# Performance work log

Hardware: AMD Instinct MI355X
Metric: run time of the kernel (lower is better)

Reference implementation:

```python
import jax, jax.numpy as jnp
import numpy as np

B_, S_, F_, N_, H_ = 4, 8192, 512, 64, 2048  # batch, seq, features, state_dim, mlp hidden
EPS = 1e-5


def setup_inputs() -> dict:
    key = jax.random.key(0)
    ks = jax.random.split(key, 24)
    F, N, H = F_, N_, H_

    def nrm(k, shape, scale=1.0):
        return jax.random.normal(k, shape, dtype=jnp.float32) * scale

    inp = {}
    inp['x'] = nrm(ks[0], (B_, S_, F))
    inp['cond'] = nrm(ks[1], (B_, F))
    n = jnp.arange(N, dtype=jnp.float32)
    for i, p in enumerate(['fwd', 'bwd']):
        b = 2 + i * 6
        inp[p + '_logAre'] = jnp.log(n + 0.5)          # HiPPO-diag: A_real = -(n+0.5)
        inp[p + '_Aim'] = jnp.pi * n                    # HiPPO-diag: A_imag = pi*n
        inp[p + '_Bre'] = nrm(ks[b], (N, F), 1.0 / np.sqrt(N))
        inp[p + '_Bim'] = nrm(ks[b + 1], (N, F), 1.0 / np.sqrt(N))
        inp[p + '_Cre'] = nrm(ks[b + 2], (F, N), 1.0 / np.sqrt(F))
        inp[p + '_Cim'] = nrm(ks[b + 3], (F, N), 1.0 / np.sqrt(F))
        inp[p + '_D'] = nrm(ks[b + 4], (F,))
        inp[p + '_logdt'] = jax.random.uniform(ks[b + 5], (N,), minval=jnp.log(0.001), maxval=jnp.log(0.1))
    inp['proj_w'] = nrm(ks[14], (2 * F, F), 1.0 / np.sqrt(2 * F))
    inp['proj_b'] = jnp.zeros((F,), jnp.float32)
    # AdaLN modulation: Dense(6F) on silu(cond); zero-init in the model, small random here
    inp['ada_w'] = nrm(ks[15], (F, 6 * F), 0.02)
    inp['ada_b'] = jnp.zeros((6 * F,), jnp.float32)
    inp['mlp_w1'] = nrm(ks[16], (F, H), 1.0 / np.sqrt(F))
    inp['mlp_b1'] = jnp.zeros((H,), jnp.float32)
    inp['mlp_w2'] = nrm(ks[17], (H, F), 1.0 / np.sqrt(H))
    inp['mlp_b2'] = jnp.zeros((F,), jnp.float32)
    return inp


def _ln(x):
    mu = jnp.mean(x, axis=-1, keepdims=True)
    v = jnp.mean(jnp.square(x - mu), axis=-1, keepdims=True)
    return (x - mu) * jax.lax.rsqrt(v + EPS)


def _s5(u, logAre, Aim, Bre, Bim, Cre, Cim, D, logdt):
    dt = jnp.exp(logdt)
    A = -jnp.exp(logAre) + 1j * Aim                       # [N] complex diagonal
    A_bar = jnp.exp(A * dt)                               # ZOH discretization
    B_bar = (A_bar[:, None] - 1.0) / (A[:, None] + 1e-8) * (Bre + 1j * Bim)  # [N,F]
    u32 = u.astype(jnp.float32)
    Bu = jnp.einsum('bsf,nf->bsn', u32, B_bar)            # [B,S,N] complex
    Ab = jnp.broadcast_to(A_bar[None, None, :], Bu.shape)

    def op(e1, e2):
        a1, b1 = e1
        a2, b2 = e2
        return (a1 * a2, a2 * b1 + b2)

    _, xs = jax.lax.associative_scan(op, (Ab, Bu), axis=1)
    y = jnp.einsum('fn,bsn->bsf', Cre + 1j * Cim, xs).real + D * u32
    return y.astype(u.dtype)


def reference(x, cond, fwd_logAre, fwd_Aim, fwd_Bre, fwd_Bim, fwd_Cre, fwd_Cim, fwd_D, fwd_logdt,
              bwd_logAre, bwd_Aim, bwd_Bre, bwd_Bim, bwd_Cre, bwd_Cim, bwd_D, bwd_logdt,
              proj_w, proj_b, ada_w, ada_b, mlp_w1, mlp_b1, mlp_w2, mlp_b2):
    mods = jax.nn.silu(cond) @ ada_w + ada_b              # [B,6F]
    sh1, sc1, g1, sh2, sc2, g2 = [m[:, None, :] for m in jnp.split(mods, 6, axis=-1)]
    h = _ln(x) * (1.0 + sc1) + sh1
    y_fwd = _s5(h, fwd_logAre, fwd_Aim, fwd_Bre, fwd_Bim, fwd_Cre, fwd_Cim, fwd_D, fwd_logdt)
    y_bwd = jnp.flip(_s5(jnp.flip(h, axis=1), bwd_logAre, bwd_Aim, bwd_Bre, bwd_Bim, bwd_Cre, bwd_Cim, bwd_D, bwd_logdt), axis=1)
    y = jnp.concatenate([y_fwd, y_bwd], axis=-1) @ proj_w + proj_b
    x = x + g1 * y
    h2 = _ln(x) * (1.0 + sc2) + sh2
    x = x + g2 * (jax.nn.gelu(h2 @ mlp_w1 + mlp_b1) @ mlp_w2 + mlp_b2)
    return x
```

## Files before the change

kernel.cpp:

```cpp
#include <hip/hip_runtime.h>
#include <hip/hip_bf16.h>

typedef unsigned short u16;
typedef __attribute__((ext_vector_type(8))) short bf16x8;
typedef __attribute__((ext_vector_type(4))) float f32x4;

#define Bc 4
#define Sc 8192
#define Fc 512
#define Nc 64
#define Hc 2048
#define Tc 32768
#define SIXF 3072

__device__ __forceinline__ u16 f2bf(float v) {
  __hip_bfloat16 h = __float2bfloat16(v);
  return *reinterpret_cast<u16*>(&h);
}
__device__ __forceinline__ float bf2f(u16 u) {
  return __uint_as_float(((unsigned)u) << 16);
}
__device__ __forceinline__ float ldf(const void* p, long i, int bf) {
  return bf ? bf2f(((const u16*)p)[i]) : ((const float*)p)[i];
}

__device__ __forceinline__ void ld16(const u16* g, u16* l) {
  __builtin_amdgcn_global_load_lds(
      (const __attribute__((address_space(1))) unsigned int*)g,
      (__attribute__((address_space(3))) unsigned int*)l,
      16, 0, 0);
}

__device__ __forceinline__ void xcd_swz(int& bx, int& by) {
  int gx = gridDim.x;
  int nwg = gx * gridDim.y;
  int lin = blockIdx.x + gx * blockIdx.y;
  if ((nwg & 7) == 0) {
    int q = nwg >> 3;
    lin = (lin & 7) * q + (lin >> 3);
  }
  bx = lin % gx;
  by = lin / gx;
}

__global__ void k_detect(const u16* __restrict__ x, int* __restrict__ flag) {
  if (threadIdx.x == 0) {
    int cnt = 0;
    for (int i = 0; i < 256; ++i) {
      int e = (x[i] >> 7) & 0xFF;
      cnt += (e >= 130);
    }
    *flag = (cnt >= 16) ? 0 : 1;
  }
}

__global__ void k_convert(const void* __restrict__ src, float* __restrict__ dst,
                          int n, const int* __restrict__ flag) {
  int bf = *flag;
  int i = blockIdx.x * blockDim.x + threadIdx.x;
  int stride = gridDim.x * blockDim.x;
  for (int j = i; j < n; j += stride) dst[j] = ldf(src, j, bf);
}

__global__ __launch_bounds__(256) void k_mods_init(const void* __restrict__ ada_b,
                                                   const int* __restrict__ flag,
                                                   float* __restrict__ mods) {
  int bf = *flag;
  int col = blockIdx.x * 256 + threadIdx.x;
  float v = ldf(ada_b, col, bf);
  for (int b = 0; b < Bc; ++b) mods[b * SIXF + col] = v;
}

__global__ __launch_bounds__(256) void k_mods2(const void* __restrict__ cond,
                                               const void* __restrict__ ada_w,
                                               const int* __restrict__ flag,
                                               float* __restrict__ mods) {
  int bf = *flag;
  int b = blockIdx.y;
  int f0 = blockIdx.z * 128;
  int col = blockIdx.x * 256 + threadIdx.x;
  __shared__ float sc[128];
  for (int i = threadIdx.x; i < 128; i += 256) {
    float c = ldf(cond, b * Fc + f0 + i, bf);
    sc[i] = c / (1.f + expf(-c));
  }
  __syncthreads();
  float acc = 0.f;
  for (int f = 0; f < 128; ++f) acc = fmaf(sc[f], ldf(ada_w, (long)(f0 + f) * SIXF + col, bf), acc);
  atomicAdd(&mods[b * SIXF + col], acc);
}

__global__ void k_prep(const void* lAf, const void* Aif, const void* Brf, const void* Bif, const void* ldtf,
                       const void* lAb, const void* Aib, const void* Brb, const void* Bib, const void* ldtb,
                       const int* __restrict__ flag,
                       u16* __restrict__ Wbup, float* __restrict__ Abar) {
  int bf = *flag;
  int dir = blockIdx.x;
  int f0 = blockIdx.y * 64;
  int n = threadIdx.x;
  const void* lA = dir ? lAb : lAf;
  const void* Ai = dir ? Aib : Aif;
  const void* Br = dir ? Brb : Brf;
  const void* Bi = dir ? Bib : Bif;
  const void* ld = dir ? ldtb : ldtf;
  float dt  = expf(ldf(ld, n, bf));
  float Are = -expf(ldf(lA, n, bf));
  float Aim = ldf(Ai, n, bf);
  float er  = expf(Are * dt);
  float abr = er * cosf(Aim * dt);
  float abi = er * sinf(Aim * dt);
  if (blockIdx.y == 0) {
    Abar[(dir * Nc + n) * 2 + 0] = abr;
    Abar[(dir * Nc + n) * 2 + 1] = abi;
  }
  float dr = Are + 1e-8f, di = Aim;
  float den = dr * dr + di * di;
  float nr = abr - 1.f, ni = abi;
  float cr = (nr * dr + ni * di) / den;
  float ci = (ni * dr - nr * di) / den;
  int col_re = dir * 128 + n, col_im = dir * 128 + 64 + n;
  for (int f = f0; f < f0 + 64; ++f) {
    float br = ldf(Br, n * Fc + f, bf), bi = ldf(Bi, n * Fc + f, bf);
    Wbup[(((f >> 3) * 256) + col_re) * 8 + (f & 7)] = f2bf(cr * br - ci * bi);
    Wbup[(((f >> 3) * 256) + col_im) * 8 + (f & 7)] = f2bf(cr * bi + ci * br);
  }
}

__global__ __launch_bounds__(256) void k_P2p(const void* Df, const void* Db, const void* pw,
                                             const int* __restrict__ flag, u16* __restrict__ P2p) {
  int bf = *flag;
  int idx = blockIdx.x * 256 + threadIdx.x;
  int f1 = idx >> 9, fo = idx & 511;
  float v = ldf(Df, f1, bf) * ldf(pw, (long)f1 * Fc + fo, bf) +
            ldf(Db, f1, bf) * ldf(pw, (long)(Fc + f1) * Fc + fo, bf);
  P2p[(((f1 >> 3) * Fc) + fo) * 8 + (f1 & 7)] = f2bf(v);
}

__global__ __launch_bounds__(256) void k_Cpm(const void* Cref, const void* Cimf,
                                             const void* Creb, const void* Cimb,
                                             const int* __restrict__ flag, u16* __restrict__ Cpm) {
  int bf = *flag;
  int k = blockIdx.x;
  int dir = k >> 7, c = (k >> 6) & 1, n = k & 63;
  const void* C = dir ? (c ? Cimb : Creb) : (c ? Cimf : Cref);
  float sgn = c ? -1.f : 1.f;
  for (int f = threadIdx.x; f < Fc; f += 256)
    Cpm[k * Fc + f] = f2bf(sgn * ldf(C, (long)f * Nc + n, bf));
}

__global__ __launch_bounds__(256) void k_Wpack(const void* __restrict__ src, const int* __restrict__ flag,
                                               int log2N, u16* __restrict__ dst) {
  int bf = *flag;
  long i = (long)blockIdx.x * 256 + threadIdx.x;
  int Nn = 1 << log2N;
  long k8 = i >> log2N;
  int n = (int)(i & (Nn - 1));
  u16 tmp[8];
#pragma unroll
  for (int j = 0; j < 8; ++j)
    tmp[j] = f2bf(ldf(src, ((k8 << 3) + j) * (long)Nn + n, bf));
  *(ushort4*)(dst + i * 8)     = *(ushort4*)tmp;
  *(ushort4*)(dst + i * 8 + 4) = *(ushort4*)(tmp + 4);
}

__global__ __launch_bounds__(256) void k_ln(const void* __restrict__ src, int srcmode,
                                            long src_tok_base, int b0,
                                            const int* __restrict__ flag,
                                            const float* __restrict__ mods,
                                            int sh_base, int sc_base,
                                            u16* __restrict__ dst) {
  int bf = srcmode ? 1 : *flag;
  long lt = blockIdx.x;
  int b = b0 + (int)(lt >> 13);
  int t = threadIdx.x;
  long si = (src_tok_base + lt) * Fc;
  float x0 = ldf(src, si + t, bf);
  float x1 = ldf(src, si + t + 256, bf);
  float s = x0 + x1, qq = x0 * x0 + x1 * x1;
  for (int o = 32; o; o >>= 1) { s += __shfl_down(s, o); qq += __shfl_down(qq, o); }
  __shared__ float ss[4], sq[4];
  int w = t >> 6;
  if ((t & 63) == 0) { ss[w] = s; sq[w] = qq; }
  __syncthreads();
  float S = ss[0] + ss[1] + ss[2] + ss[3];
  float Q = sq[0] + sq[1] + sq[2] + sq[3];
  float mu = S * (1.f / Fc);
  float var = Q * (1.f / Fc) - mu * mu;
  float rs = rsqrtf(var + 1e-5f);
  const float* mb = mods + b * SIXF;
  float h0 = (x0 - mu) * rs * (1.f + mb[sc_base + t]) + mb[sh_base + t];
  float h1 = (x1 - mu) * rs * (1.f + mb[sc_base + t + 256]) + mb[sh_base + t + 256];
  dst[lt * Fc + t] = f2bf(h0);
  dst[lt * Fc + t + 256] = f2bf(h1);
}

struct Smem { u16 As[2][128 * 64]; u16 Ws[2][64 * 128]; };

__device__ __forceinline__ int mfma_gemm(Smem& sm, int cur,
                                         const u16* __restrict__ A, long row0, int K,
                                         const u16* __restrict__ Wp, int N, int col0,
                                         f32x4 (&acc)[4][4]) {
  const int tid = threadIdx.x;
  const int l = tid & 63;
  const int q = l >> 4, li = l & 15;
  const int w = tid >> 6;
  const int wm = (w >> 1) << 6, wn = (w & 1) << 6;
  const int m0 = tid >> 3;
  const int kc0 = (tid & 7) ^ (m0 & 7);
  const long aoff0 = (row0 + m0) * (long)K + (kc0 << 3);
  const long woff0 = (long)(tid >> 7) * ((long)N << 3) + ((long)(col0 + (tid & 127)) << 3);
  const int lbase = w << 9;
  const int T = K >> 6;

  auto stage = [&](int buf, int k0) {
#pragma unroll
    for (int it = 0; it < 4; ++it)
      ld16(A + aoff0 + (long)it * ((long)K << 5) + k0, sm.As[buf] + lbase + (it << 11));
#pragma unroll
    for (int it = 0; it < 4; ++it)
      ld16(Wp + woff0 + (long)k0 * N + (long)it * ((long)N << 4), sm.Ws[buf] + lbase + (it << 11));
  };

  stage(cur, 0);
  asm volatile("s_waitcnt vmcnt(0)" ::: "memory");
  __builtin_amdgcn_s_barrier();
  __builtin_amdgcn_sched_barrier(0);

  for (int t = 0; t < T; ++t) {
    if (t + 1 < T) stage(cur ^ 1, (t + 1) << 6);
    const u16* As = sm.As[cur];
    const u16* Ws = sm.Ws[cur];
#pragma unroll
    for (int ks = 0; ks < 2; ++ks) {
      bf16x8 af[4], bw[4];
#pragma unroll
      for (int mt = 0; mt < 4; ++mt) {
        int mrow = wm + (mt << 4) + li;
        af[mt] = *(const bf16x8*)(As + (((mrow << 3) + (((ks << 2) + q) ^ (mrow & 7))) << 3));
      }
#pragma unroll
      for (int nt = 0; nt < 4; ++nt) {
        int n = wn + (nt << 4) + li;
        bw[nt] = *(const bf16x8*)(Ws + ((((((ks << 2) + q) << 7) + n)) << 3));
      }
#pragma unroll
      for (int mt = 0; mt < 4; ++mt)
#pragma unroll
        for (int nt = 0; nt < 4; ++nt)
          acc[mt][nt] = __builtin_amdgcn_mfma_f32_16x16x32_bf16(af[mt], bw[nt], acc[mt][nt], 0, 0, 0);
    }
    if (t + 1 < T) {
      asm volatile("s_waitcnt vmcnt(0)" ::: "memory");
      __builtin_amdgcn_s_barrier();
      __builtin_amdgcn_sched_barrier(0);
    }
    cur ^= 1;
  }
  return cur;
}

__global__ __launch_bounds__(256) void k_Gp2(const u16* __restrict__ Cpm, const u16* __restrict__ pwp,
                                             u16* __restrict__ Gp) {
  __shared__ Smem sm;
  f32x4 acc[4][4] = {};
  int bx, by; xcd_swz(bx, by);
  long row0 = (long)by * 128;
  int col0 = bx << 7;
  int dir = (int)(row0 >> 7);
  mfma_gemm(sm, 0, Cpm, row0, Fc, pwp + (size_t)dir * 262144, Fc, col0, acc);
  const int l = threadIdx.x & 63, q = l >> 4, li = l & 15;
  const int w = threadIdx.x >> 6;
  const int wm = (w >> 1) << 6, wn = (w & 1) << 6;
#pragma unroll
  for (int mt = 0; mt < 4; ++mt)
#pragma unroll
    for (int nt = 0; nt < 4; ++nt)
#pragma unroll
      for (int r = 0; r < 4; ++r) {
        int k = (int)row0 + wm + (mt << 4) + (q << 2) + r;
        int col = col0 + wn + (nt << 4) + li;
        Gp[(((k >> 3) * Fc) + col) * 8 + (k & 7)] = f2bf(acc[mt][nt][r]);
      }
}

__global__ __launch_bounds__(256) void k_gemm_bu(const u16* __restrict__ h,
                                                 const u16* __restrict__ Wbup,
                                                 int nb, float* __restrict__ Bu) {
  __shared__ Smem sm;
  f32x4 acc[4][4] = {};
  int bx, by; xcd_swz(bx, by);
  long row0 = (long)by * 128;
  int col0 = bx << 7;
  mfma_gemm(sm, 0, h, row0, Fc, Wbup, 256, col0, acc);
  const int l = threadIdx.x & 63, q = l >> 4, li = l & 15;
  const int w = threadIdx.x >> 6;
  const int wm = (w >> 1) << 6, wn = (w & 1) << 6;
#pragma unroll
  for (int mt = 0; mt < 4; ++mt) {
#pragma unroll
    for (int nt = 0; nt < 4; ++nt) {
      int col = col0 + wn + (nt << 4) + li;
      int dir = col >> 7, cc = (col >> 6) & 1, n = col & 63;
#pragma unroll
      for (int r = 0; r < 4; ++r) {
        long lt = row0 + wm + (mt << 4) + (q << 2) + r;
        int lb = (int)(lt >> 13), s = (int)(lt & 8191);
        int spos = dir ? (Sc - 1 - s) : s;
        Bu[((((long)dir * nb + lb) * Nc + n) * Sc + spos) * 2 + cc] = acc[mt][nt][r];
      }
    }
  }
}

__global__ __launch_bounds__(256) void k_scan(float* __restrict__ Bu, const float* __restrict__ Abar,
                                              int nb) {
  int blk = blockIdx.x;
  int per_dir = nb * 64;
  int dir = blk / per_dir;
  int rem = blk - dir * per_dir;
  int lb = rem >> 6, n = rem & 63;
  float ar = Abar[(dir * Nc + n) * 2 + 0];
  float ai = Abar[(dir * Nc + n) * 2 + 1];
  float* base = Bu + (((long)dir * nb + lb) * Nc + n) * Sc * 2;
  int t = threadIdx.x;
  float4 loc[16];
  float lr = 0.f, li = 0.f;
  const float4* bp = (const float4*)base + t * 16;
#pragma unroll
  for (int j = 0; j < 16; ++j) {
    float4 v = bp[j];
    loc[j] = v;
    float nr = fmaf(ar, lr, fmaf(-ai, li, v.x));
    float ni = fmaf(ar, li, fmaf(ai, lr, v.y));
    lr = fmaf(ar, nr, fmaf(-ai, ni, v.z));
    li = fmaf(ar, ni, fmaf(ai, nr, v.w));
  }
  __shared__ float sr[256], si[256];
  float pr = ar, pi = ai;
  for (int k = 0; k < 5; ++k) { float t2 = pr * pr - pi * pi; pi = 2.f * pr * pi; pr = t2; }
  float vr = lr, vi = li;
  for (int step = 1; step < 256; step <<= 1) {
    sr[t] = vr; si[t] = vi;
    __syncthreads();
    if (t >= step) {
      float orr = sr[t - step], oii = si[t - step];
      vr = vr + pr * orr - pi * oii;
      vi = vi + pr * oii + pi * orr;
    }
    __syncthreads();
    float t2 = pr * pr - pi * pi; pi = 2.f * pr * pi; pr = t2;
  }
  sr[t] = vr; si[t] = vi;
  __syncthreads();
  float xr = (t == 0) ? 0.f : sr[t - 1];
  float xi = (t == 0) ? 0.f : si[t - 1];
  float4* op = (float4*)base + t * 16;
#pragma unroll
  for (int j = 0; j < 16; ++j) {
    float4 v = loc[j];
    float nr = fmaf(ar, xr, fmaf(-ai, xi, v.x));
    float ni = fmaf(ar, xi, fmaf(ai, xr, v.y));
    xr = fmaf(ar, nr, fmaf(-ai, ni, v.z));
    xi = fmaf(ar, ni, fmaf(ai, nr, v.w));
    float4 o; o.x = nr; o.y = ni; o.z = xr; o.w = xi;
    op[j] = o;
  }
}

__global__ __launch_bounds__(256) void k_xs_t(const float* __restrict__ xs, int nb,
                                              u16* __restrict__ xh, u16* __restrict__ xl) {
  __shared__ float tile[32 * 257];
  long t0 = (long)blockIdx.x * 32;
  int lb = (int)(t0 >> 13);
  int s0 = (int)(t0 & 8191);
  int tid = threadIdx.x;
  int ls = tid & 31;
  int half = (tid >> 5) & 1;
  int wv = tid >> 6;
#pragma unroll 4
  for (int cg = 0; cg < 32; ++cg) {
    int col = cg * 8 + wv * 2 + half;
    int dir = col >> 7, cc = (col >> 6) & 1, n = col & 63;
    int spos = dir ? (Sc - 1 - (s0 + ls)) : (s0 + ls);
    float v = xs[((((long)dir * nb + lb) * Nc + n) * Sc + spos) * 2 + cc];
    tile[ls * 257 + col] = v;
  }
  __syncthreads();
  for (int j = 0; j < 32; ++j) {
    float v = tile[j * 257 + tid];
    u16 hi = f2bf(v);
    long lt = t0 + j;
    xh[lt * 256 + tid] = hi;
    xl[lt * 256 + tid] = f2bf(v - bf2f(hi));
  }
}

__global__ __launch_bounds__(256) void k_gemm_y(const u16* __restrict__ xh, const u16* __restrict__ xl,
                                                const u16* __restrict__ Gp,
                                                const u16* __restrict__ h, const u16* __restrict__ P2p,
                                                const void* __restrict__ xraw, long tok_base, int b0,
                                                const int* __restrict__ flag,
                                                const float* __restrict__ mods, const float* __restrict__ pb,
                                                u16* __restrict__ out1) {
  __shared__ Smem sm;
  f32x4 acc[4][4] = {};
  int bx, by; xcd_swz(bx, by);
  long row0 = (long)by * 128;
  int col0 = bx << 7;
  int cur = 0;
  cur = mfma_gemm(sm, cur, xh, row0, 256, Gp, Fc, col0, acc);
  cur = mfma_gemm(sm, cur, xl, row0, 256, Gp, Fc, col0, acc);
  cur = mfma_gemm(sm, cur, h, row0, Fc, P2p, Fc, col0, acc);
  int bf = *flag;
  const int l = threadIdx.x & 63, q = l >> 4, li = l & 15;
  const int w = threadIdx.x >> 6;
  const int wm = (w >> 1) << 6, wn = (w & 1) << 6;
#pragma unroll
  for (int mt = 0; mt < 4; ++mt) {
#pragma unroll
    for (int r = 0; r < 4; ++r) {
      long lt = row0 + wm + (mt << 4) + (q << 2) + r;
      int b = b0 + (int)(lt >> 13);
      const float* mb = mods + b * SIXF + 2 * Fc;
#pragma unroll
      for (int nt = 0; nt < 4; ++nt) {
        int col = col0 + wn + (nt << 4) + li;
        float xv = ldf(xraw, (tok_base + lt) * Fc + col, bf);
        out1[lt * Fc + col] = f2bf(xv + mb[col] * (acc[mt][nt][r] + pb[col]));
      }
    }
  }
}

__device__ __forceinline__ float gelu_t(float u) {
  float z = 0.7978845608028654f * fmaf(0.044715f * u * u, u, u);
  float e = __builtin_amdgcn_exp2f(z * -2.8853900817779268f);
  return u * __builtin_amdgcn_rcpf(1.f + e);
}

__global__ __launch_bounds__(256) void k_mlp1(const u16* __restrict__ h2, const u16* __restrict__ W1p,
                                              const float* __restrict__ b1, long crow0,
                                              u16* __restrict__ tbuf) {
  __shared__ Smem sm;
  f32x4 acc[4][4] = {};
  int bx, by; xcd_swz(bx, by);
  long row0 = crow0 + (long)by * 128;
  int col0 = bx << 7;
  mfma_gemm(sm, 0, h2, row0, Fc, W1p, Hc, col0, acc);
  const int l = threadIdx.x & 63, q = l >> 4, li = l & 15;
  const int w = threadIdx.x >> 6;
  const int wm = (w >> 1) << 6, wn = (w & 1) << 6;
#pragma unroll
  for (int mt = 0; mt < 4; ++mt) {
#pragma unroll
    for (int r = 0; r < 4; ++r) {
      long lr2 = row0 - crow0 + wm + (mt << 4) + (q << 2) + r;
#pragma unroll
      for (int nt = 0; nt < 4; ++nt) {
        int col = col0 + wn + (nt << 4) + li;
        tbuf[lr2 * Hc + col] = f2bf(gelu_t(acc[mt][nt][r] + b1[col]));
      }
    }
  }
}

__global__ __launch_bounds__(256) void k_mlp2(const u16* __restrict__ tbuf, const u16* __restrict__ W2p,
                                              const float* __restrict__ b2, const u16* __restrict__ out1,
                                              const float* __restrict__ mods, long crow0,
                                              long tok_base, int b0,
                                              const int* __restrict__ flag, void* __restrict__ dout) {
  __shared__ Smem sm;
  f32x4 acc[4][4] = {};
  int bx, by; xcd_swz(bx, by);
  long lrow0 = (long)by * 128;
  int col0 = bx << 7;
  mfma_gemm(sm, 0, tbuf, lrow0, Hc, W2p, Fc, col0, acc);
  int bf = *flag;
  const int l = threadIdx.x & 63, q = l >> 4, li = l & 15;
  const int w = threadIdx.x >> 6;
  const int wm = (w >> 1) << 6, wn = (w & 1) << 6;
#pragma unroll
  for (int mt = 0; mt < 4; ++mt) {
#pragma unroll
    for (int r = 0; r < 4; ++r) {
      long lt = crow0 + lrow0 + wm + (mt << 4) + (q << 2) + r;
      int b = b0 + (int)(lt >> 13);
      const float* mb = mods + b * SIXF + 5 * Fc;
#pragma unroll
      for (int nt = 0; nt < 4; ++nt) {
        int col = col0 + wn + (nt << 4) + li;
        float v = bf2f(out1[lt * Fc + col]) + mb[col] * (acc[mt][nt][r] + b2[col]);
        long oi = (tok_base + lt) * Fc + col;
        if (bf) ((u16*)dout)[oi] = f2bf(v);
        else    ((float*)dout)[oi] = v;
      }
    }
  }
}

extern "C" void kernel_launch(void* const* d_in, const int* in_sizes, int n_in,
                              void* d_out, int out_size, void* d_ws, size_t ws_size,
                              hipStream_t stream) {
  char* ws = (char*)d_ws;
  size_t off = 0;
  auto alloc = [&](size_t bytes) -> char* {
    char* p = ws + off;
    off += (bytes + 255) & ~(size_t)255;
    return p;
  };
  int*   flag = (int*)  alloc(4);
  float* mods = (float*)alloc((size_t)Bc * SIXF * 4);
  float* Abar = (float*)alloc(2 * Nc * 2 * 4);
  float* pbf  = (float*)alloc(Fc * 4);
  float* b1f  = (float*)alloc(Hc * 4);
  float* b2f  = (float*)alloc(Fc * 4);
  u16* Wbup = (u16*)alloc((size_t)Fc * 256 * 2);
  u16* Gp   = (u16*)alloc((size_t)256 * Fc * 2);
  u16* P2p  = (u16*)alloc((size_t)Fc * Fc * 2);
  u16* W1p  = (u16*)alloc((size_t)Fc * Hc * 2);
  u16* W2p  = (u16*)alloc((size_t)Hc * Fc * 2);
  u16* pwp  = (u16*)alloc((size_t)1024 * Fc * 2);
  u16* Cpm  = (u16*)alloc((size_t)256 * Fc * 2);
  size_t off_static = off;

  const size_t U = (size_t)Sc * Fc * 2;
  int nb = 4;
  while (nb > 1 && off_static + (size_t)nb * 4 * U + 4096 > ws_size) nb >>= 1;

  u16*   h    = (u16*)  alloc((size_t)nb * U);
  float* Bu   = (float*)alloc((size_t)nb * U);
  u16*   xh   = (u16*)  alloc((size_t)nb * U / 2);
  u16*   xl   = (u16*)  alloc((size_t)nb * U / 2);
  u16*   out1 = (u16*)  alloc((size_t)nb * U);
  u16* tch = (u16*)Bu;
  u16* h2  = h;

  k_detect<<<1, 64, 0, stream>>>((const u16*)d_in[0], flag);
  k_convert<<<2, 256, 0, stream>>>(d_in[19], pbf, Fc, flag);
  k_convert<<<8, 256, 0, stream>>>(d_in[23], b1f, Hc, flag);
  k_convert<<<2, 256, 0, stream>>>(d_in[25], b2f, Fc, flag);
  k_mods_init<<<12, 256, 0, stream>>>(d_in[21], flag, mods);
  k_mods2<<<dim3(12, Bc, 4), 256, 0, stream>>>(d_in[1], d_in[20], flag, mods);
  k_prep<<<dim3(2, 8), 64, 0, stream>>>(d_in[2], d_in[3], d_in[4], d_in[5], d_in[9],
                                        d_in[10], d_in[11], d_in[12], d_in[13], d_in[17],
                                        flag, Wbup, Abar);
  k_P2p<<<(Fc * Fc) / 256, 256, 0, stream>>>(d_in[8], d_in[16], d_in[18], flag, P2p);
  k_Wpack<<<256, 256, 0, stream>>>(d_in[18], flag, 9, pwp);
  k_Cpm<<<256, 256, 0, stream>>>(d_in[6], d_in[7], d_in[14], d_in[15], flag, Cpm);
  k_Gp2<<<dim3(4, 2), 256, 0, stream>>>(Cpm, pwp, Gp);
  k_Wpack<<<512, 256, 0, stream>>>(d_in[22], flag, 11, W1p);
  k_Wpack<<<512, 256, 0, stream>>>(d_in[24], flag, 9, W2p);

  for (int b0 = 0; b0 < Bc; b0 += nb) {
    long tok_base = (long)b0 * Sc;
    long rows = (long)nb * Sc;
    k_ln<<<rows, 256, 0, stream>>>(d_in[0], 0, tok_base, b0, flag, mods, 0, Fc, h);
    k_gemm_bu<<<dim3(2, rows / 128), 256, 0, stream>>>(h, Wbup, nb, Bu);
    k_scan<<<2 * nb * 64, 256, 0, stream>>>(Bu, Abar, nb);
    k_xs_t<<<rows / 32, 256, 0, stream>>>(Bu, nb, xh, xl);
    k_gemm_y<<<dim3(Fc / 128, rows / 128), 256, 0, stream>>>(xh, xl, Gp, h, P2p,
                                                             d_in[0], tok_base, b0, flag, mods, pbf, out1);
    k_ln<<<rows, 256, 0, stream>>>(out1, 1, 0, b0, flag, mods, 3 * Fc, 4 * Fc, h2);
    long RC = rows / 2;
    for (int ch = 0; ch < 2; ++ch) {
      long crow0 = ch * RC;
      k_mlp1<<<dim3(Hc / 128, RC / 128), 256, 0, stream>>>(h2, W1p, b1f, crow0, tch);
      k_mlp2<<<dim3(Fc / 128, RC / 128), 256, 0, stream>>>(tch, W2p, b2f, out1, mods, crow0,
                                                           tok_base, b0, flag, d_out);
    }
  }
  (void)n_in; (void)out_size; (void)in_sizes;
}
```

Before: 639.5 us.

## Fuse y-GEMM operands into one K=1024 GEMM and use 256x256 tiles

The xs hi/lo split and the LN output h are packed into one interleaved activation buffer [xh|xl|h] with row stride 1024. The three y-projection weights are packed into a single K=1024 weight, so k_gemm_y becomes one GEMM. k_gemm_y and k_mlp1 switch to 512-thread blocks with 256x256 tiles to increase operand reuse per load. The GEMM pipeline now issues the next stage's loads before waiting with a partial vmcnt and adds s_setprio around the MFMAs. The larger tiles use more LDS and registers, which may lower occupancy or leave too few blocks per wave.

```diff
diff --git a/kernel.cpp b/kernel.cpp
--- a/kernel.cpp
+++ b/kernel.cpp
@@ -10,7 +10,6 @@
 #define Fc 512
 #define Nc 64
 #define Hc 2048
-#define Tc 32768
 #define SIXF 3072
 
 __device__ __forceinline__ u16 f2bf(float v) {
@@ -127,13 +126,13 @@
 }
 
 __global__ __launch_bounds__(256) void k_P2p(const void* Df, const void* Db, const void* pw,
-                                             const int* __restrict__ flag, u16* __restrict__ P2p) {
+                                             const int* __restrict__ flag, u16* __restrict__ Wyp) {
   int bf = *flag;
   int idx = blockIdx.x * 256 + threadIdx.x;
   int f1 = idx >> 9, fo = idx & 511;
   float v = ldf(Df, f1, bf) * ldf(pw, (long)f1 * Fc + fo, bf) +
             ldf(Db, f1, bf) * ldf(pw, (long)(Fc + f1) * Fc + fo, bf);
-  P2p[(((f1 >> 3) * Fc) + fo) * 8 + (f1 & 7)] = f2bf(v);
+  Wyp[((((f1 >> 3) + 64) * Fc) + fo) * 8 + (f1 & 7)] = f2bf(v);
 }
 
 __global__ __launch_bounds__(256) void k_Cpm(const void* Cref, const void* Cimf,
@@ -168,7 +167,7 @@
                                             const int* __restrict__ flag,
                                             const float* __restrict__ mods,
                                             int sh_base, int sc_base,
-                                            u16* __restrict__ dst) {
+                                            u16* __restrict__ dst, int ldd, int dcol) {
   int bf = srcmode ? 1 : *flag;
   long lt = blockIdx.x;
   int b = b0 + (int)(lt >> 13);
@@ -190,44 +189,45 @@
   const float* mb = mods + b * SIXF;
   float h0 = (x0 - mu) * rs * (1.f + mb[sc_base + t]) + mb[sh_base + t];
   float h1 = (x1 - mu) * rs * (1.f + mb[sc_base + t + 256]) + mb[sh_base + t + 256];
-  dst[lt * Fc + t] = f2bf(h0);
-  dst[lt * Fc + t + 256] = f2bf(h1);
-}
-
-struct Smem { u16 As[2][128 * 64]; u16 Ws[2][64 * 128]; };
-
-__device__ __forceinline__ int mfma_gemm(Smem& sm, int cur,
-                                         const u16* __restrict__ A, long row0, int K,
-                                         const u16* __restrict__ Wp, int N, int col0,
-                                         f32x4 (&acc)[4][4]) {
+  dst[lt * (long)ldd + dcol + t] = f2bf(h0);
+  dst[lt * (long)ldd + dcol + t + 256] = f2bf(h1);
+}
+
+struct SmemA { u16 As[2][128 * 64]; u16 Ws[2][64 * 128]; };
+
+__device__ __forceinline__ void mfma_gemm128(SmemA& sm, const u16* __restrict__ A, long row0,
+                                             int lda, int K,
+                                             const u16* __restrict__ Wp, int N, int col0,
+                                             f32x4 (&acc)[4][4]) {
   const int tid = threadIdx.x;
-  const int l = tid & 63;
-  const int q = l >> 4, li = l & 15;
+  const int l = tid & 63, q = l >> 4, li = l & 15;
   const int w = tid >> 6;
   const int wm = (w >> 1) << 6, wn = (w & 1) << 6;
   const int m0 = tid >> 3;
   const int kc0 = (tid & 7) ^ (m0 & 7);
-  const long aoff0 = (row0 + m0) * (long)K + (kc0 << 3);
+  const long aoff0 = (row0 + m0) * (long)lda + (kc0 << 3);
   const long woff0 = (long)(tid >> 7) * ((long)N << 3) + ((long)(col0 + (tid & 127)) << 3);
-  const int lbase = w << 9;
+  const int lb = w << 9;
   const int T = K >> 6;
-
+  int cur = 0;
   auto stage = [&](int buf, int k0) {
 #pragma unroll
     for (int it = 0; it < 4; ++it)
-      ld16(A + aoff0 + (long)it * ((long)K << 5) + k0, sm.As[buf] + lbase + (it << 11));
+      ld16(A + aoff0 + (long)it * ((long)lda << 5) + k0, sm.As[buf] + (it << 11) + lb);
 #pragma unroll
     for (int it = 0; it < 4; ++it)
-      ld16(Wp + woff0 + (long)k0 * N + (long)it * ((long)N << 4), sm.Ws[buf] + lbase + (it << 11));
+      ld16(Wp + woff0 + (long)k0 * N + (long)it * ((long)N << 4), sm.Ws[buf] + (it << 11) + lb);
   };
-
-  stage(cur, 0);
-  asm volatile("s_waitcnt vmcnt(0)" ::: "memory");
-  __builtin_amdgcn_s_barrier();
-  __builtin_amdgcn_sched_barrier(0);
-
+  stage(0, 0);
   for (int t = 0; t < T; ++t) {
-    if (t + 1 < T) stage(cur ^ 1, (t + 1) << 6);
+    if (t + 1 < T) {
+      stage(cur ^ 1, (t + 1) << 6);
+      asm volatile("s_waitcnt vmcnt(8)" ::: "memory");
+    } else {
+      asm volatile("s_waitcnt vmcnt(0)" ::: "memory");
+    }
+    __builtin_amdgcn_s_barrier();
+    __builtin_amdgcn_sched_barrier(0);
     const u16* As = sm.As[cur];
     const u16* Ws = sm.Ws[cur];
 #pragma unroll
@@ -241,7 +241,7 @@
 #pragma unroll
       for (int nt = 0; nt < 4; ++nt) {
         int n = wn + (nt << 4) + li;
-        bw[nt] = *(const bf16x8*)(Ws + ((((((ks << 2) + q) << 7) + n)) << 3));
+        bw[nt] = *(const bf16x8*)(Ws + (((((ks << 2) + q) << 7) | n) << 3));
       }
 #pragma unroll
       for (int mt = 0; mt < 4; ++mt)
@@ -249,25 +249,83 @@
         for (int nt = 0; nt < 4; ++nt)
           acc[mt][nt] = __builtin_amdgcn_mfma_f32_16x16x32_bf16(af[mt], bw[nt], acc[mt][nt], 0, 0, 0);
     }
+    __builtin_amdgcn_s_barrier();
+    __builtin_amdgcn_sched_barrier(0);
+    cur ^= 1;
+  }
+}
+
+struct SmemB { u16 As[2][256 * 64]; u16 Ws[2][64 * 256]; };
+
+__device__ __forceinline__ void mfma_gemm256(SmemB& sm, const u16* __restrict__ A, long row0,
+                                             int lda, int K,
+                                             const u16* __restrict__ Wp, int N, int col0,
+                                             f32x4 (&acc)[8][4]) {
+  const int tid = threadIdx.x;
+  const int l = tid & 63, q = l >> 4, li = l & 15;
+  const int w = tid >> 6;
+  const int wm = (w >> 2) << 7, wn = (w & 3) << 6;
+  const int m0 = tid >> 3;
+  const int kc0 = (tid & 7) ^ (m0 & 7);
+  const long aoff0 = (row0 + m0) * (long)lda + (kc0 << 3);
+  const long woff0 = (long)(tid >> 8) * ((long)N << 3) + ((long)(col0 + (tid & 255)) << 3);
+  const int lb = w << 9;
+  const int T = K >> 6;
+  int cur = 0;
+  auto stage = [&](int buf, int k0) {
+#pragma unroll
+    for (int it = 0; it < 4; ++it)
+      ld16(A + aoff0 + (long)it * ((long)lda << 6) + k0, sm.As[buf] + (it << 12) + lb);
+#pragma unroll
+    for (int it = 0; it < 4; ++it)
+      ld16(Wp + woff0 + (long)k0 * N + (long)it * ((long)N << 4), sm.Ws[buf] + (it << 12) + lb);
+  };
+  stage(0, 0);
+  for (int t = 0; t < T; ++t) {
     if (t + 1 < T) {
+      stage(cur ^ 1, (t + 1) << 6);
+      asm volatile("s_waitcnt vmcnt(8)" ::: "memory");
+    } else {
       asm volatile("s_waitcnt vmcnt(0)" ::: "memory");
-      __builtin_amdgcn_s_barrier();
-      __builtin_amdgcn_sched_barrier(0);
-    }
+    }
+    __builtin_amdgcn_s_barrier();
+    __builtin_amdgcn_sched_barrier(0);
+    const u16* As = sm.As[cur];
+    const u16* Ws = sm.Ws[cur];
+    __builtin_amdgcn_s_setprio(1);
+#pragma unroll
+    for (int ks = 0; ks < 2; ++ks) {
+      bf16x8 bw[4];
+#pragma unroll
+      for (int nt = 0; nt < 4; ++nt) {
+        int n = wn + (nt << 4) + li;
+        bw[nt] = *(const bf16x8*)(Ws + (((((ks << 2) + q) << 8) | n) << 3));
+      }
+#pragma unroll
+      for (int mt = 0; mt < 8; ++mt) {
+        int mrow = wm + (mt << 4) + li;
+        bf16x8 af = *(const bf16x8*)(As + (((mrow << 3) + (((ks << 2) + q) ^ (mrow & 7))) << 3));
+#pragma unroll
+        for (int nt = 0; nt < 4; ++nt)
+          acc[mt][nt] = __builtin_amdgcn_mfma_f32_16x16x32_bf16(af, bw[nt], acc[mt][nt], 0, 0, 0);
+      }
+    }
+    __builtin_amdgcn_s_setprio(0);
+    __builtin_amdgcn_s_barrier();
+    __builtin_amdgcn_sched_barrier(0);
     cur ^= 1;
   }
-  return cur;
 }
 
 __global__ __launch_bounds__(256) void k_Gp2(const u16* __restrict__ Cpm, const u16* __restrict__ pwp,
-                                             u16* __restrict__ Gp) {
-  __shared__ Smem sm;
+                                             u16* __restrict__ Wyp) {
+  __shared__ SmemA sm;
   f32x4 acc[4][4] = {};
   int bx, by; xcd_swz(bx, by);
   long row0 = (long)by * 128;
   int col0 = bx << 7;
   int dir = (int)(row0 >> 7);
-  mfma_gemm(sm, 0, Cpm, row0, Fc, pwp + (size_t)dir * 262144, Fc, col0, acc);
+  mfma_gemm128(sm, Cpm, row0, Fc, Fc, pwp + (size_t)dir * 262144, Fc, col0, acc);
   const int l = threadIdx.x & 63, q = l >> 4, li = l & 15;
   const int w = threadIdx.x >> 6;
   const int wm = (w >> 1) << 6, wn = (w & 1) << 6;
@@ -279,19 +337,22 @@
       for (int r = 0; r < 4; ++r) {
         int k = (int)row0 + wm + (mt << 4) + (q << 2) + r;
         int col = col0 + wn + (nt << 4) + li;
-        Gp[(((k >> 3) * Fc) + col) * 8 + (k & 7)] = f2bf(acc[mt][nt][r]);
-      }
-}
-
-__global__ __launch_bounds__(256) void k_gemm_bu(const u16* __restrict__ h,
+        u16 v = f2bf(acc[mt][nt][r]);
+        size_t i0 = (((size_t)(k >> 3)) * Fc + col) * 8 + (k & 7);
+        Wyp[i0] = v;
+        Wyp[i0 + (size_t)32 * Fc * 8] = v;
+      }
+}
+
+__global__ __launch_bounds__(256) void k_gemm_bu(const u16* __restrict__ hp,
                                                  const u16* __restrict__ Wbup,
                                                  int nb, float* __restrict__ Bu) {
-  __shared__ Smem sm;
+  __shared__ SmemA sm;
   f32x4 acc[4][4] = {};
   int bx, by; xcd_swz(bx, by);
   long row0 = (long)by * 128;
   int col0 = bx << 7;
-  mfma_gemm(sm, 0, h, row0, Fc, Wbup, 256, col0, acc);
+  mfma_gemm128(sm, hp, row0, 1024, Fc, Wbup, 256, col0, acc);
   const int l = threadIdx.x & 63, q = l >> 4, li = l & 15;
   const int w = threadIdx.x >> 6;
   const int wm = (w >> 1) << 6, wn = (w & 1) << 6;
@@ -368,7 +429,7 @@
 }
 
 __global__ __launch_bounds__(256) void k_xs_t(const float* __restrict__ xs, int nb,
-                                              u16* __restrict__ xh, u16* __restrict__ xl) {
+                                              u16* __restrict__ hxl) {
   __shared__ float tile[32 * 257];
   long t0 = (long)blockIdx.x * 32;
   int lb = (int)(t0 >> 13);
@@ -390,33 +451,30 @@
     float v = tile[j * 257 + tid];
     u16 hi = f2bf(v);
     long lt = t0 + j;
-    xh[lt * 256 + tid] = hi;
-    xl[lt * 256 + tid] = f2bf(v - bf2f(hi));
-  }
-}
-
-__global__ __launch_bounds__(256) void k_gemm_y(const u16* __restrict__ xh, const u16* __restrict__ xl,
-                                                const u16* __restrict__ Gp,
-                                                const u16* __restrict__ h, const u16* __restrict__ P2p,
-                                                const void* __restrict__ xraw, long tok_base, int b0,
-                                                const int* __restrict__ flag,
-                                                const float* __restrict__ mods, const float* __restrict__ pb,
-                                                u16* __restrict__ out1) {
-  __shared__ Smem sm;
-  f32x4 acc[4][4] = {};
+    hxl[lt * 1024 + tid] = hi;
+    hxl[lt * 1024 + 256 + tid] = f2bf(v - bf2f(hi));
+  }
+}
+
+__global__ __launch_bounds__(512, 2) void k_gemm_y(const u16* __restrict__ hxl,
+                                                   const u16* __restrict__ Wyp,
+                                                   const void* __restrict__ xraw, long tok_base, int b0,
+                                                   const int* __restrict__ flag,
+                                                   const float* __restrict__ mods,
+                                                   const float* __restrict__ pb,
+                                                   u16* __restrict__ out1) {
+  __shared__ SmemB sm;
+  f32x4 acc[8][4] = {};
   int bx, by; xcd_swz(bx, by);
-  long row0 = (long)by * 128;
-  int col0 = bx << 7;
-  int cur = 0;
-  cur = mfma_gemm(sm, cur, xh, row0, 256, Gp, Fc, col0, acc);
-  cur = mfma_gemm(sm, cur, xl, row0, 256, Gp, Fc, col0, acc);
-  cur = mfma_gemm(sm, cur, h, row0, Fc, P2p, Fc, col0, acc);
+  long row0 = (long)by << 8;
+  int col0 = bx << 8;
+  mfma_gemm256(sm, hxl, row0, 1024, 1024, Wyp, Fc, col0, acc);
   int bf = *flag;
   const int l = threadIdx.x & 63, q = l >> 4, li = l & 15;
   const int w = threadIdx.x >> 6;
-  const int wm = (w >> 1) << 6, wn = (w & 1) << 6;
-#pragma unroll
-  for (int mt = 0; mt < 4; ++mt) {
+  const int wm = (w >> 2) << 7, wn = (w & 3) << 6;
+#pragma unroll
+  for (int mt = 0; mt < 8; ++mt) {
 #pragma unroll
     for (int r = 0; r < 4; ++r) {
       long lt = row0 + wm + (mt << 4) + (q << 2) + r;
@@ -438,20 +496,20 @@
   return u * __builtin_amdgcn_rcpf(1.f + e);
 }
 
-__global__ __launch_bounds__(256) void k_mlp1(const u16* __restrict__ h2, const u16* __restrict__ W1p,
-                                              const float* __restrict__ b1, long crow0,
-                                              u16* __restrict__ tbuf) {
-  __shared__ Smem sm;
-  f32x4 acc[4][4] = {};
+__global__ __launch_bounds__(512, 2) void k_mlp1(const u16* __restrict__ h2, const u16* __restrict__ W1p,
+                                                 const float* __restrict__ b1, long crow0,
+                                                 u16* __restrict__ tbuf) {
+  __shared__ SmemB sm;
+  f32x4 acc[8][4] = {};
   int bx, by; xcd_swz(bx, by);
-  long row0 = crow0 + (long)by * 128;
-  int col0 = bx << 7;
-  mfma_gemm(sm, 0, h2, row0, Fc, W1p, Hc, col0, acc);
+  long row0 = crow0 + ((long)by << 8);
+  int col0 = bx << 8;
+  mfma_gemm256(sm, h2, row0, Fc, Fc, W1p, Hc, col0, acc);
   const int l = threadIdx.x & 63, q = l >> 4, li = l & 15;
   const int w = threadIdx.x >> 6;
-  const int wm = (w >> 1) << 6, wn = (w & 1) << 6;
-#pragma unroll
-  for (int mt = 0; mt < 4; ++mt) {
+  const int wm = (w >> 2) << 7, wn = (w & 3) << 6;
+#pragma unroll
+  for (int mt = 0; mt < 8; ++mt) {
 #pragma unroll
     for (int r = 0; r < 4; ++r) {
       long lr2 = row0 - crow0 + wm + (mt << 4) + (q << 2) + r;
@@ -469,12 +527,12 @@
                                               const float* __restrict__ mods, long crow0,
                                               long tok_base, int b0,
                                               const int* __restrict__ flag, void* __restrict__ dout) {
-  __shared__ Smem sm;
+  __shared__ SmemA sm;
   f32x4 acc[4][4] = {};
   int bx, by; xcd_swz(bx, by);
   long lrow0 = (long)by * 128;
   int col0 = bx << 7;
-  mfma_gemm(sm, 0, tbuf, lrow0, Hc, W2p, Fc, col0, acc);
+  mfma_gemm128(sm, tbuf, lrow0, Hc, Hc, W2p, Fc, col0, acc);
   int bf = *flag;
   const int l = threadIdx.x & 63, q = l >> 4, li = l & 15;
   const int w = threadIdx.x >> 6;
@@ -515,8 +573,7 @@
   float* b1f  = (float*)alloc(Hc * 4);
   float* b2f  = (float*)alloc(Fc * 4);
   u16* Wbup = (u16*)alloc((size_t)Fc * 256 * 2);
-  u16* Gp   = (u16*)alloc((size_t)256 * Fc * 2);
-  u16* P2p  = (u16*)alloc((size_t)Fc * Fc * 2);
+  u16* Wyp  = (u16*)alloc((size_t)128 * Fc * 8 * 2);
   u16* W1p  = (u16*)alloc((size_t)Fc * Hc * 2);
   u16* W2p  = (u16*)alloc((size_t)Hc * Fc * 2);
   u16* pwp  = (u16*)alloc((size_t)1024 * Fc * 2);
@@ -527,13 +584,11 @@
   int nb = 4;
   while (nb > 1 && off_static + (size_t)nb * 4 * U + 4096 > ws_size) nb >>= 1;
 
-  u16*   h    = (u16*)  alloc((size_t)nb * U);
+  u16*   hxl  = (u16*)  alloc((size_t)nb * U * 2);
   float* Bu   = (float*)alloc((size_t)nb * U);
-  u16*   xh   = (u16*)  alloc((size_t)nb * U / 2);
-  u16*   xl   = (u16*)  alloc((size_t)nb * U / 2);
   u16*   out1 = (u16*)  alloc((size_t)nb * U);
-  u16* tch = (u16*)Bu;
-  u16* h2  = h;
+  u16* tch = hxl;
+  u16* h2  = (u16*)Bu;
 
   k_detect<<<1, 64, 0, stream>>>((const u16*)d_in[0], flag);
   k_convert<<<2, 256, 0, stream>>>(d_in[19], pbf, Fc, flag);
@@ -544,29 +599,29 @@
   k_prep<<<dim3(2, 8), 64, 0, stream>>>(d_in[2], d_in[3], d_in[4], d_in[5], d_in[9],
                                         d_in[10], d_in[11], d_in[12], d_in[13], d_in[17],
                                         flag, Wbup, Abar);
-  k_P2p<<<(Fc * Fc) / 256, 256, 0, stream>>>(d_in[8], d_in[16], d_in[18], flag, P2p);
+  k_P2p<<<(Fc * Fc) / 256, 256, 0, stream>>>(d_in[8], d_in[16], d_in[18], flag, Wyp);
   k_Wpack<<<256, 256, 0, stream>>>(d_in[18], flag, 9, pwp);
   k_Cpm<<<256, 256, 0, stream>>>(d_in[6], d_in[7], d_in[14], d_in[15], flag, Cpm);
-  k_Gp2<<<dim3(4, 2), 256, 0, stream>>>(Cpm, pwp, Gp);
+  k_Gp2<<<dim3(4, 2), 256, 0, stream>>>(Cpm, pwp, Wyp);
   k_Wpack<<<512, 256, 0, stream>>>(d_in[22], flag, 11, W1p);
   k_Wpack<<<512, 256, 0, stream>>>(d_in[24], flag, 9, W2p);
 
   for (int b0 = 0; b0 < Bc; b0 += nb) {
     long tok_base = (long)b0 * Sc;
     long rows = (long)nb * Sc;
-    k_ln<<<rows, 256, 0, stream>>>(d_in[0], 0, tok_base, b0, flag, mods, 0, Fc, h);
-    k_gemm_bu<<<dim3(2, rows / 128), 256, 0, stream>>>(h, Wbup, nb, Bu);
+    k_ln<<<rows, 256, 0, stream>>>(d_in[0], 0, tok_base, b0, flag, mods, 0, Fc, hxl, 1024, 512);
+    k_gemm_bu<<<dim3(2, rows / 128), 256, 0, stream>>>(hxl + 512, Wbup, nb, Bu);
     k_scan<<<2 * nb * 64, 256, 0, stream>>>(Bu, Abar, nb);
-    k_xs_t<<<rows / 32, 256, 0, stream>>>(Bu, nb, xh, xl);
-    k_gemm_y<<<dim3(Fc / 128, rows / 128), 256, 0, stream>>>(xh, xl, Gp, h, P2p,
-                                                             d_in[0], tok_base, b0, flag, mods, pbf, out1);
-    k_ln<<<rows, 256, 0, stream>>>(out1, 1, 0, b0, flag, mods, 3 * Fc, 4 * Fc, h2);
+    k_xs_t<<<rows / 32, 256, 0, stream>>>(Bu, nb, hxl);
+    k_gemm_y<<<dim3(2, rows / 256), 512, 0, stream>>>(hxl, Wyp, d_in[0], tok_base, b0,
+                                                      flag, mods, pbf, out1);
+    k_ln<<<rows, 256, 0, stream>>>(out1, 1, 0, b0, flag, mods, 3 * Fc, 4 * Fc, h2, 512, 0);
     long RC = rows / 2;
     for (int ch = 0; ch < 2; ++ch) {
       long crow0 = ch * RC;
-      k_mlp1<<<dim3(Hc / 128, RC / 128), 256, 0, stream>>>(h2, W1p, b1f, crow0, tch);
-      k_mlp2<<<dim3(Fc / 128, RC / 128), 256, 0, stream>>>(tch, W2p, b2f, out1, mods, crow0,
-                                                           tok_base, b0, flag, d_out);
+      k_mlp1<<<dim3(8, RC / 256), 512, 0, stream>>>(h2, W1p, b1f, crow0, tch);
+      k_mlp2<<<dim3(4, RC / 128), 256, 0, stream>>>(tch, W2p, b2f, out1, mods, crow0,
+                                                    tok_base, b0, flag, d_out);
     }
   }
   (void)n_in; (void)out_size; (void)in_sizes;
```

Result: faster. 623.5 us (-2.5%).
